# Kernel optimization log

Hardware: AMD Instinct MI355X
Metric: run time of the kernel (lower is better)

The kernel has to match this reference:

```python
import jax, jax.numpy as jnp
import numpy as np

N = 13627        # n_nodes (from negative_sampling call in source)
E_EDGES = 504378 # n_edges
F_IN = 64
H1, H2, LIN_H = 300, 100, 100  # CONFIG HIDDEN_1/HIDDEN_2/LINEAR_HIDDEN


def setup_inputs() -> dict:
    key = jax.random.key(0)
    ks = jax.random.split(key, 10)
    x = jax.random.normal(ks[0], (N, F_IN), jnp.float32)
    edge_index = jax.random.randint(ks[1], (2, E_EDGES), 0, N, dtype=jnp.int64)
    neg_edge_index = jax.random.randint(ks[2], (2, E_EDGES), 0, N, dtype=jnp.int64)
    def w(k, shape):
        return jax.random.normal(k, shape, jnp.float32) * 0.05
    return dict(
        x=x, edge_index=edge_index, neg_edge_index=neg_edge_index,
        W1=w(ks[3], (2, F_IN, H1)), b1=jnp.zeros((H1,), jnp.float32),
        W2=w(ks[4], (2, H1, H2)), b2=jnp.zeros((H2,), jnp.float32),
        W3=w(ks[5], (2, H2, 1)), b3=jnp.zeros((1,), jnp.float32),
        linW1=w(ks[6], (F_IN, LIN_H)), linb1=jnp.zeros((LIN_H,), jnp.float32),
        linW2=w(ks[7], (F_IN, LIN_H)), linb2=jnp.zeros((LIN_H,), jnp.float32),
        c1=jnp.array([0.5], jnp.float32), c2=jnp.array([0.5], jnp.float32),
    )


def _cheb_norm(edge_index, n):
    # PyG ChebConv sym normalization with lambda_max=2: Lhat = L - I,
    # off-diagonal entries -deg[src]^-1/2 * deg[dst]^-1/2, diagonal 0.
    src, dst = edge_index[0], edge_index[1]
    deg = jax.ops.segment_sum(jnp.ones(src.shape, jnp.float32), src, num_segments=n)
    dinv = jnp.where(deg > 0, jax.lax.rsqrt(jnp.maximum(deg, 1.0)), 0.0)
    return -dinv[src] * dinv[dst]


def _cheb_conv(x, W, b, src, dst, norm, n):
    # K=2: out = Tx0 @ W[0] + Tx1 @ W[1] + b, with Tx1 = Lhat @ x (gather-scale-scatter)
    tx1 = jax.ops.segment_sum(norm[:, None] * x[src], dst, num_segments=n)
    return x @ W[0] + tx1 @ W[1] + b


def reference(x, edge_index, neg_edge_index, W1, b1, W2, b2, W3, b3,
              linW1, linb1, linW2, linb2, c1, c2):
    n = x.shape[0]
    src, dst = edge_index[0], edge_index[1]
    norm = _cheb_norm(edge_index, n)
    h = jax.nn.relu(_cheb_conv(x, W1, b1, src, dst, norm, n))
    x1 = jax.nn.relu(_cheb_conv(h, W2, b2, src, dst, norm, n))
    xo = x1 + jax.nn.relu(x @ linW1 + linb1)
    z = x1 + jax.nn.relu(x @ linW2 + linb2)
    pos = jax.nn.sigmoid(jnp.sum(z[edge_index[0]] * z[edge_index[1]], axis=1))
    pos_loss = -jnp.mean(jnp.log(pos + 1e-15))
    neg = jax.nn.sigmoid(jnp.sum(z[neg_edge_index[0]] * z[neg_edge_index[1]], axis=1))
    neg_loss = -jnp.mean(jnp.log(1.0 - neg + 1e-15))
    r_loss = pos_loss + neg_loss
    out = _cheb_conv(xo, W3, b3, src, dst, norm, n)
    return out, r_loss, c1, c2
```

## Files before the change

### kernel.cpp

```cpp
#include <hip/hip_runtime.h>
#include <math.h>


typedef unsigned short ushort_t;
typedef float v2f __attribute__((ext_vector_type(2)));
typedef short bf16x8 __attribute__((ext_vector_type(8)));
typedef float f32x4 __attribute__((ext_vector_type(4)));

#define GBM 64
#define GBN 64
#define GBK 32
#define LDK 72
#define HB  256
#define PACKN 6816

__device__ inline short f2bf(float f) {
    unsigned u = __float_as_uint(f);
    u += 0x7fff + ((u >> 16) & 1);
    return (short)(u >> 16);
}
__device__ inline float bflo(unsigned w) { return __uint_as_float(w << 16); }
__device__ inline float bfhi(unsigned w) { return __uint_as_float(w & 0xffff0000u); }

__device__ inline float dot16fp8(uint4 ra, uint4 rb) {
    float dot = 0.0f;
    v2f fa, fb;
    fa = __builtin_amdgcn_cvt_pk_f32_fp8(ra.x, false);
    fb = __builtin_amdgcn_cvt_pk_f32_fp8(rb.x, false);
    dot += fa.x * fb.x + fa.y * fb.y;
    fa = __builtin_amdgcn_cvt_pk_f32_fp8(ra.x, true);
    fb = __builtin_amdgcn_cvt_pk_f32_fp8(rb.x, true);
    dot += fa.x * fb.x + fa.y * fb.y;
    fa = __builtin_amdgcn_cvt_pk_f32_fp8(ra.y, false);
    fb = __builtin_amdgcn_cvt_pk_f32_fp8(rb.y, false);
    dot += fa.x * fb.x + fa.y * fb.y;
    fa = __builtin_amdgcn_cvt_pk_f32_fp8(ra.y, true);
    fb = __builtin_amdgcn_cvt_pk_f32_fp8(rb.y, true);
    dot += fa.x * fb.x + fa.y * fb.y;
    fa = __builtin_amdgcn_cvt_pk_f32_fp8(ra.z, false);
    fb = __builtin_amdgcn_cvt_pk_f32_fp8(rb.z, false);
    dot += fa.x * fb.x + fa.y * fb.y;
    fa = __builtin_amdgcn_cvt_pk_f32_fp8(ra.z, true);
    fb = __builtin_amdgcn_cvt_pk_f32_fp8(rb.z, true);
    dot += fa.x * fb.x + fa.y * fb.y;
    fa = __builtin_amdgcn_cvt_pk_f32_fp8(ra.w, false);
    fb = __builtin_amdgcn_cvt_pk_f32_fp8(rb.w, false);
    dot += fa.x * fb.x + fa.y * fb.y;
    fa = __builtin_amdgcn_cvt_pk_f32_fp8(ra.w, true);
    fb = __builtin_amdgcn_cvt_pk_f32_fp8(rb.w, true);
    dot += fa.x * fb.x + fa.y * fb.y;
    return dot;
}

__global__ __launch_bounds__(512) void hist_both_pairs_kernel(
    const int* __restrict__ ei, const int* __restrict__ nei,
    int* __restrict__ degp, int* __restrict__ cntp,
    int2* __restrict__ pp, int2* __restrict__ pn, int E) {
    __shared__ int lhs[PACKN];
    __shared__ int lhd[PACKN];
    for (int i = threadIdx.x; i < PACKN; i += 512) { lhs[i] = 0; lhd[i] = 0; }
    __syncthreads();
    const int b = blockIdx.x;
    const int chunk = (E + HB - 1) / HB;
    const int e0 = b * chunk;
    const int e1 = (e0 + chunk < E) ? (e0 + chunk) : E;
    for (int e = e0 + threadIdx.x; e < e1; e += 512) {
        int s = ei[e], d = ei[E + e];
        atomicAdd(&lhs[s >> 1], 1 << ((s & 1) << 4));
        atomicAdd(&lhd[d >> 1], 1 << ((d & 1) << 4));
        pp[e] = make_int2(s, d);
        pn[e] = make_int2(nei[e], nei[E + e]);
    }
    __syncthreads();
    int* ds = degp + (size_t)b * PACKN;
    int* cs = cntp + (size_t)b * PACKN;
    for (int i = threadIdx.x; i < PACKN; i += 512) { ds[i] = lhs[i]; cs[i] = lhd[i]; }
}

__global__ void merge_kernel(const int* __restrict__ degp, const int* __restrict__ cntp,
                             ushort_t* __restrict__ off, int Nal,
                             float* __restrict__ dinv, int* __restrict__ rowptr,
                             float* __restrict__ acc, int n) {
    int v = blockIdx.x * blockDim.x + threadIdx.x;
    if (v == 0) {
        rowptr[0] = 0;
        acc[0] = 0.0f; acc[1] = 0.0f; acc[2] = 0.0f; acc[3] = 0.0f;
    }
    if (v >= n) return;
    const int vh = v >> 1, sh = (v & 1) << 4;
    int d = 0;
    for (int b = 0; b < HB; ++b)
        d += (degp[(size_t)b * PACKN + vh] >> sh) & 0xffff;
    dinv[v] = (d > 0) ? (1.0f / sqrtf((float)d)) : 0.0f;
    int run = 0;
    for (int b = 0; b < HB; ++b) {
        off[(size_t)b * Nal + v] = (ushort_t)run;
        run += (cntp[(size_t)b * PACKN + vh] >> sh) & 0xffff;
    }
    rowptr[v + 1] = run;
}

__global__ void scan_kernel(int* __restrict__ rowptr, int n) {
    __shared__ int wsum[16];
    __shared__ int carry_s;
    if (threadIdx.x == 0) carry_s = 0;
    __syncthreads();
    int nchunk = (n + 1023) / 1024;
    int wid = threadIdx.x >> 6, lane = threadIdx.x & 63;
    for (int c = 0; c < nchunk; ++c) {
        int i = c * 1024 + threadIdx.x;
        int v = (i < n) ? rowptr[i + 1] : 0;
        int s = v;
        for (int off = 1; off < 64; off <<= 1) {
            int t = __shfl_up(s, off, 64);
            if (lane >= off) s += t;
        }
        if (lane == 63) wsum[wid] = s;
        __syncthreads();
        if (wid == 0 && lane < 16) {
            int wsv = wsum[lane];
            for (int off = 1; off < 16; off <<= 1) {
                int t = __shfl_up(wsv, off, 64);
                if (lane >= off) wsv += t;
            }
            wsum[lane] = wsv;
        }
        __syncthreads();
        int base = carry_s + (wid > 0 ? wsum[wid - 1] : 0);
        int inc = base + s;
        if (i < n) rowptr[i + 1] = inc;
        __syncthreads();
        if (threadIdx.x == 1023) carry_s = inc;
        __syncthreads();
    }
}

__global__ __launch_bounds__(512) void fill_lds_kernel(
    const int* __restrict__ ei, const float* __restrict__ dinv,
    const int* __restrict__ rowptr, const ushort_t* __restrict__ off, int Nal,
    int* __restrict__ colidx, float* __restrict__ wnorm, int E) {
    __shared__ int lh[PACKN];
    for (int i = threadIdx.x; i < PACKN; i += 512) lh[i] = 0;
    __syncthreads();
    const int b = blockIdx.x;
    const int chunk = (E + HB - 1) / HB;
    const int e0 = b * chunk;
    const int e1 = (e0 + chunk < E) ? (e0 + chunk) : E;
    const ushort_t* boff = off + (size_t)b * Nal;
    for (int e = e0 + threadIdx.x; e < e1; e += 512) {
        int s = ei[e], d = ei[E + e];
        int sh = (d & 1) << 4;
        int old = atomicAdd(&lh[d >> 1], 1 << sh);
        int rank = (old >> sh) & 0xffff;
        int slot = rowptr[d] + (int)boff[d] + rank;
        colidx[slot] = s;
        wnorm[slot] = -dinv[s] * dinv[d];
    }
}

__global__ void xt_kernel(const float* __restrict__ x, const int* __restrict__ rowptr,
                          const int* __restrict__ colidx, const float* __restrict__ wnorm,
                          float* __restrict__ XT, int n) {
    int node = (blockIdx.x * blockDim.x + threadIdx.x) >> 6;
    if (node >= n) return;
    int lane = threadIdx.x & 63;
    int grp = lane >> 4;
    int l = lane & 15;
    int j0 = rowptr[node], j1 = rowptr[node + 1];
    float4 a = {0, 0, 0, 0};
    int j = j0 + grp;
    if (j < j1) {
        float w = wnorm[j];
        int c = colidx[j];
        float4 r = ((const float4*)(x + (size_t)c * 64))[l];
        for (;;) {
            int jn = j + 4;
            bool more = jn < j1;
            float wn = 0.0f;
            float4 rn = r;
            if (more) {
                int cn = colidx[jn];
                wn = wnorm[jn];
                rn = ((const float4*)(x + (size_t)cn * 64))[l];
            }
            a.x += w * r.x; a.y += w * r.y; a.z += w * r.z; a.w += w * r.w;
            if (!more) break;
            j = jn; w = wn; r = rn;
        }
    }
#pragma unroll
    for (int off = 16; off <= 32; off <<= 1) {
        a.x += __shfl_xor(a.x, off, 64);
        a.y += __shfl_xor(a.y, off, 64);
        a.z += __shfl_xor(a.z, off, 64);
        a.w += __shfl_xor(a.w, off, 64);
    }
    if (grp == 0) {
        float4 xv = ((const float4*)(x + (size_t)node * 64))[l];
        *(float4*)&XT[(size_t)node * 128 + l * 4] = xv;
        *(float4*)&XT[(size_t)node * 128 + 64 + l * 4] = a;
    }
}

__global__ __launch_bounds__(256) void gemm_mfma(
    const float* __restrict__ A, int lda,
    const float* __restrict__ B0, const float* __restrict__ B1,
    const float* __restrict__ bias0, const float* __restrict__ bias1,
    float* __restrict__ C, int ldc, ushort_t* __restrict__ Cbf,
    int Nrows, int K, int Ncols, int split, int relu) {
    __shared__ short As[GBM * LDK];
    __shared__ short Bs[GBN * LDK];
    const int bm = blockIdx.y * GBM, bn = blockIdx.x * GBN;
    const int tid = threadIdx.x;
    const int w = tid >> 6, l = tid & 63;
    const int wm = (w >> 1) * 32, wn = (w & 1) * 32;
    const int lr = l & 15;
    const int kg = l >> 4;
    const int arow = tid >> 2, aseg = tid & 3;
    const int bcol = tid & 63, bk2 = (tid >> 6) * 2;
    const int ldb0 = split, ldb1 = Ncols - split;

    const int arowg = bm + arow;
    const int bcolg = bn + bcol;
    const float* Bsrc = (bcolg < split) ? (B0 + bcolg)
                       : ((bcolg < Ncols) ? (B1 + (bcolg - split)) : nullptr);
    const int ldb = (bcolg < split) ? ldb0 : ldb1;

    f32x4 acc00 = {0,0,0,0}, acc01 = {0,0,0,0}, acc10 = {0,0,0,0}, acc11 = {0,0,0,0};

    for (int k0 = 0; k0 < K; k0 += GBK) {
        {
            int kk = k0 + aseg * 8;
            bf16x8 v;
            if (arowg < Nrows && kk + 7 < K) {
                float4 f0 = *(const float4*)&A[(size_t)arowg * lda + kk];
                float4 f1 = *(const float4*)&A[(size_t)arowg * lda + kk + 4];
                v[0] = f2bf(f0.x); v[1] = f2bf(f0.y); v[2] = f2bf(f0.z); v[3] = f2bf(f0.w);
                v[4] = f2bf(f1.x); v[5] = f2bf(f1.y); v[6] = f2bf(f1.z); v[7] = f2bf(f1.w);
            } else {
#pragma unroll
                for (int i = 0; i < 8; ++i)
                    v[i] = (arowg < Nrows && kk + i < K)
                         ? f2bf(A[(size_t)arowg * lda + kk + i]) : (short)0;
            }
            *(bf16x8*)&As[arow * LDK + aseg * 8] = v;
        }
#pragma unroll
        for (int q = 0; q < 4; ++q) {
            int k = q * 8 + bk2;
            unsigned pw = 0u;
            if (Bsrc) {
                float f0 = (k0 + k < K) ? Bsrc[(size_t)(k0 + k) * ldb] : 0.0f;
                float f1 = (k0 + k + 1 < K) ? Bsrc[(size_t)(k0 + k + 1) * ldb] : 0.0f;
                pw = (unsigned)(unsigned short)f2bf(f0)
                   | ((unsigned)(unsigned short)f2bf(f1) << 16);
            }
            *(unsigned*)&Bs[bcol * LDK + k] = pw;
        }
        __syncthreads();
        bf16x8 a0 = *(const bf16x8*)&As[(wm + lr) * LDK + kg * 8];
        bf16x8 a1 = *(const bf16x8*)&As[(wm + 16 + lr) * LDK + kg * 8];
        bf16x8 b0 = *(const bf16x8*)&Bs[(wn + lr) * LDK + kg * 8];
        bf16x8 b1 = *(const bf16x8*)&Bs[(wn + 16 + lr) * LDK + kg * 8];
        acc00 = __builtin_amdgcn_mfma_f32_16x16x32_bf16(a0, b0, acc00, 0, 0, 0);
        acc01 = __builtin_amdgcn_mfma_f32_16x16x32_bf16(a0, b1, acc01, 0, 0, 0);
        acc10 = __builtin_amdgcn_mfma_f32_16x16x32_bf16(a1, b0, acc10, 0, 0, 0);
        acc11 = __builtin_amdgcn_mfma_f32_16x16x32_bf16(a1, b1, acc11, 0, 0, 0);
        __syncthreads();
    }
#pragma unroll
    for (int i = 0; i < 2; ++i) {
        int rbase = bm + wm + i * 16 + kg * 4;
#pragma unroll
        for (int j = 0; j < 2; ++j) {
            int col = bn + wn + j * 16 + lr;
            if (col >= Ncols) continue;
            float bv = (col < split) ? (bias0 ? bias0[col] : 0.0f)
                                     : (bias1 ? bias1[col - split] : 0.0f);
            f32x4 a = (i == 0) ? (j == 0 ? acc00 : acc01) : (j == 0 ? acc10 : acc11);
#pragma unroll
            for (int r = 0; r < 4; ++r) {
                int row = rbase + r;
                if (row >= Nrows) continue;
                float o = a[r] + bv;
                if (relu) o = fmaxf(o, 0.0f);
                if (col < split || !Cbf)
                    C[(size_t)row * ldc + col] = o;
                else
                    Cbf[(size_t)row * 128 + (col - split)] = (ushort_t)f2bf(o);
            }
        }
    }
}

__global__ void segsum_combine1_kernel(const ushort_t* __restrict__ hb,
                                       const int* __restrict__ rowptr, const int* __restrict__ colidx,
                                       const float* __restrict__ wnorm,
                                       const float* __restrict__ G2a, const float* __restrict__ b2,
                                       float* __restrict__ x1, int n) {
    int node = (blockIdx.x * blockDim.x + threadIdx.x) >> 6;
    if (node >= n) return;
    int lane = threadIdx.x & 63;
    int grp = lane >> 4;
    int l = lane & 15;
    int j0 = rowptr[node], j1 = rowptr[node + 1];
    float acc[8] = {};
    int j = j0 + grp;
    if (j < j1) {
        float w = wnorm[j];
        int c = colidx[j];
        uint4 r = ((const uint4*)(hb + (size_t)c * 128))[l];
        for (;;) {
            int jn = j + 4;
            bool more = jn < j1;
            float wn = 0.0f;
            uint4 rn = r;
            if (more) {
                int cn = colidx[jn];
                wn = wnorm[jn];
                rn = ((const uint4*)(hb + (size_t)cn * 128))[l];
            }
            acc[0] += w * bflo(r.x); acc[1] += w * bfhi(r.x);
            acc[2] += w * bflo(r.y); acc[3] += w * bfhi(r.y);
            acc[4] += w * bflo(r.z); acc[5] += w * bfhi(r.z);
            acc[6] += w * bflo(r.w); acc[7] += w * bfhi(r.w);
            if (!more) break;
            j = jn; w = wn; r = rn;
        }
    }
#pragma unroll
    for (int k = 0; k < 8; ++k) {
        acc[k] += __shfl_xor(acc[k], 16, 64);
        acc[k] += __shfl_xor(acc[k], 32, 64);
    }
    if (grp == 0) {
        int f = l * 8;
        if (f < 100) {
            float4 g0 = *(const float4*)&G2a[(size_t)node * 100 + f];
            float4 bv0 = *(const float4*)&b2[f];
            float4 o0;
            o0.x = fmaxf(g0.x + acc[0] + bv0.x, 0.0f);
            o0.y = fmaxf(g0.y + acc[1] + bv0.y, 0.0f);
            o0.z = fmaxf(g0.z + acc[2] + bv0.z, 0.0f);
            o0.w = fmaxf(g0.w + acc[3] + bv0.w, 0.0f);
            *(float4*)&x1[(size_t)node * 100 + f] = o0;
            if (f + 8 <= 100) {
                float4 g1 = *(const float4*)&G2a[(size_t)node * 100 + f + 4];
                float4 bv1 = *(const float4*)&b2[f + 4];
                float4 o1;
                o1.x = fmaxf(g1.x + acc[4] + bv1.x, 0.0f);
                o1.y = fmaxf(g1.y + acc[5] + bv1.y, 0.0f);
                o1.z = fmaxf(g1.z + acc[6] + bv1.z, 0.0f);
                o1.w = fmaxf(g1.w + acc[7] + bv1.w, 0.0f);
                *(float4*)&x1[(size_t)node * 100 + f + 4] = o1;
            }
        }
    }
}

__global__ void combine2_kernel(const float* __restrict__ S, const float* __restrict__ x1,
                                const float* __restrict__ w3b,
                                float* __restrict__ xo, unsigned* __restrict__ zf,
                                float* __restrict__ sv, int n) {
    int idx = blockIdx.x * blockDim.x + threadIdx.x;
    if (idx >= n * 32) return;
    int i = idx >> 5, q = idx & 31;
    unsigned w = 0u;
    float part = 0.0f;
    if (q < 25) {
        float4 s1 = *(const float4*)&S[(size_t)i * 200 + q * 4];
        float4 s2 = *(const float4*)&S[(size_t)i * 200 + 100 + q * 4];
        float4 xv = *(const float4*)&x1[(size_t)i * 100 + q * 4];
        float4 a, b;
        a.x = xv.x + fmaxf(s1.x, 0.0f); a.y = xv.y + fmaxf(s1.y, 0.0f);
        a.z = xv.z + fmaxf(s1.z, 0.0f); a.w = xv.w + fmaxf(s1.w, 0.0f);
        b.x = xv.x + fmaxf(s2.x, 0.0f); b.y = xv.y + fmaxf(s2.y, 0.0f);
        b.z = xv.z + fmaxf(s2.z, 0.0f); b.w = xv.w + fmaxf(s2.w, 0.0f);
        *(float4*)&xo[(size_t)i * 100 + q * 4] = a;
        w = (unsigned)__builtin_amdgcn_cvt_pk_fp8_f32(b.x, b.y, 0, false);
        w = (unsigned)__builtin_amdgcn_cvt_pk_fp8_f32(b.z, b.w, (int)w, true);
        float4 wv = *(const float4*)&w3b[q * 4];
        part = a.x * wv.x + a.y * wv.y + a.z * wv.z + a.w * wv.w;
    }
    zf[(size_t)i * 32 + q] = w;
#pragma unroll
    for (int off = 16; off > 0; off >>= 1)
        part += __shfl_xor(part, off, 32);
    if (q == 0) sv[i] = part;
}

__global__ __launch_bounds__(256) void edge_loss_fp8_kernel(
    const unsigned* __restrict__ zf, const int2* __restrict__ pp,
    const int2* __restrict__ pn, int E, float* __restrict__ accv) {
    const int y = blockIdx.y;
    const int2* __restrict__ pairs = y ? pn : pp;
    const int l = threadIdx.x & 7;
    const int g = (blockIdx.x * blockDim.x + threadIdx.x) >> 3;
    const int ng = (gridDim.x * blockDim.x) >> 3;
    const int stride2 = 2 * ng;
    float s = 0.0f;
    const int gA = g, gB = g + ng;
    int niterA = (gA < E) ? ((E - 1 - gA) / stride2 + 1) : 0;
    int niterB = (gB < E) ? ((E - 1 - gB) / stride2 + 1) : 0;
    if (niterA > 0) {
        int eB0 = (gB < E) ? gB : (E - 1);
        int eA1 = (gA + stride2 < E) ? (gA + stride2) : (E - 1);
        int eB1 = (gB + stride2 < E) ? (gB + stride2) : (E - 1);
        int2 pA0 = pairs[gA], pB0 = pairs[eB0];
        int2 pA1 = pairs[eA1], pB1 = pairs[eB1];
        uint4 raA = *(const uint4*)&zf[(size_t)pA0.x * 32 + l * 4];
        uint4 rbA = *(const uint4*)&zf[(size_t)pA0.y * 32 + l * 4];
        uint4 raB = *(const uint4*)&zf[(size_t)pB0.x * 32 + l * 4];
        uint4 rbB = *(const uint4*)&zf[(size_t)pB0.y * 32 + l * 4];
        for (int t = 0; t < niterA; ++t) {
            int eA2 = gA + (t + 2) * stride2; eA2 = (eA2 < E) ? eA2 : (E - 1);
            int eB2 = gB + (t + 2) * stride2; eB2 = (eB2 < E) ? eB2 : (E - 1);
            int2 pA2 = pairs[eA2], pB2 = pairs[eB2];
            uint4 raA1 = *(const uint4*)&zf[(size_t)pA1.x * 32 + l * 4];
            uint4 rbA1 = *(const uint4*)&zf[(size_t)pA1.y * 32 + l * 4];
            uint4 raB1 = *(const uint4*)&zf[(size_t)pB1.x * 32 + l * 4];
            uint4 rbB1 = *(const uint4*)&zf[(size_t)pB1.y * 32 + l * 4];
            float dA = dot16fp8(raA, rbA);
            float dB = dot16fp8(raB, rbB);
            dA += __shfl_xor(dA, 1, 8); dB += __shfl_xor(dB, 1, 8);
            dA += __shfl_xor(dA, 2, 8); dB += __shfl_xor(dB, 2, 8);
            dA += __shfl_xor(dA, 4, 8); dB += __shfl_xor(dB, 4, 8);
            if (l == 0) {
                float sgA = 1.0f / (1.0f + expf(-dA));
                s += y ? logf(1.0f - sgA + 1e-15f) : logf(sgA + 1e-15f);
                if (t < niterB) {
                    float sgB = 1.0f / (1.0f + expf(-dB));
                    s += y ? logf(1.0f - sgB + 1e-15f) : logf(sgB + 1e-15f);
                }
            }
            pA1 = pA2; pB1 = pB2;
            raA = raA1; rbA = rbA1; raB = raB1; rbB = rbB1;
        }
    }
    __shared__ float red[256];
    red[threadIdx.x] = s;
    __syncthreads();
    for (int st = 128; st > 0; st >>= 1) {
        if (threadIdx.x < st) red[threadIdx.x] += red[threadIdx.x + st];
        __syncthreads();
    }
    if (threadIdx.x == 0) atomicAdd(&accv[y], red[0]);
}

__global__ void out_finalize_kernel(const float* __restrict__ xo, const float* __restrict__ W3,
                                    const float* __restrict__ b3, const int* __restrict__ rowptr,
                                    const int* __restrict__ colidx, const float* __restrict__ wnorm,
                                    const float* __restrict__ sv, const float* __restrict__ accv,
                                    const float* __restrict__ c1, const float* __restrict__ c2,
                                    float* __restrict__ out, int n, int E) {
    int i = blockIdx.x * blockDim.x + threadIdx.x;
    if (i == 0) {
        out[n]     = -(accv[0] + accv[1]) / (float)E;
        out[n + 1] = c1[0];
        out[n + 2] = c2[0];
    }
    if (i >= n) return;
    const float4* a = (const float4*)(xo + (size_t)i * 100);
    const float4* wv = (const float4*)W3;
    float acc = b3[0];
#pragma unroll
    for (int q = 0; q < 25; ++q) {
        float4 va = a[q], vw = wv[q];
        acc += va.x * vw.x + va.y * vw.y + va.z * vw.z + va.w * vw.w;
    }
    int j1 = rowptr[i + 1];
    for (int j = rowptr[i]; j < j1; ++j)
        acc += wnorm[j] * sv[colidx[j]];
    out[i] = acc;
}

extern "C" void kernel_launch(void* const* d_in, const int* in_sizes, int n_in,
                              void* d_out, int out_size, void* d_ws, size_t ws_size,
                              hipStream_t stream) {
    (void)n_in; (void)out_size; (void)ws_size;
    const float* x   = (const float*)d_in[0];
    const int*   ei  = (const int*)d_in[1];
    const int*   nei = (const int*)d_in[2];
    const float* W1  = (const float*)d_in[3];
    const float* b1  = (const float*)d_in[4];
    const float* W2  = (const float*)d_in[5];
    const float* b2  = (const float*)d_in[6];
    const float* W3  = (const float*)d_in[7];
    const float* b3  = (const float*)d_in[8];
    const float* lw1 = (const float*)d_in[9];
    const float* lb1 = (const float*)d_in[10];
    const float* lw2 = (const float*)d_in[11];
    const float* lb2 = (const float*)d_in[12];
    const float* c1  = (const float*)d_in[13];
    const float* c2  = (const float*)d_in[14];

    const int Nn = in_sizes[0] / 64;
    const int E  = in_sizes[1] / 2;

    const size_t Nal = ((size_t)Nn + 5) & ~(size_t)3;
    const size_t Eal = ((size_t)E + 3) & ~(size_t)3;

    float* ws       = (float*)d_ws;
    float* acc      = ws;
    float* dinv     = acc + 4;
    int*   rowptr   = (int*)(dinv + Nal);
    int*   colidx   = rowptr + Nal;
    float* wnorm    = (float*)(colidx + Eal);
    int2*  pp       = (int2*)(wnorm + Eal);
    int2*  pn       = pp + Eal;
    int*   degp     = (int*)(pn + Eal);
    int*   cntp     = degp + (size_t)HB * PACKN;
    ushort_t* offus = (ushort_t*)(cntp + (size_t)HB * PACKN);
    float* XT       = (float*)(offus + (size_t)HB * Nal);
    float* h        = XT + (size_t)Nn * 128;
    float* G2a      = h  + (size_t)Nn * 300;
    float* x1       = G2a + (size_t)Nn * 100;
    float* xo       = x1 + (size_t)Nn * 100;
    size_t zoff     = (size_t)(xo + (size_t)Nn * 100 - ws);
    zoff = (zoff + 31) & ~(size_t)31;
    unsigned* zf    = (unsigned*)(ws + zoff);
    size_t hoff     = zoff + (size_t)Nn * 32 + 63;
    hoff &= ~(size_t)63;
    ushort_t* hWb   = (ushort_t*)(ws + hoff);
    float* sv       = ws + hoff + (size_t)Nn * 64;
    float* S        = h;

    const int MB = (Nn + GBM - 1) / GBM;

    hist_both_pairs_kernel<<<HB, 512, 0, stream>>>(ei, nei, degp, cntp, pp, pn, E);
    merge_kernel<<<(Nn + 255) / 256, 256, 0, stream>>>(degp, cntp, offus, (int)Nal,
                                                       dinv, rowptr, acc, Nn);
    scan_kernel<<<1, 1024, 0, stream>>>(rowptr, Nn);
    fill_lds_kernel<<<HB, 512, 0, stream>>>(ei, dinv, rowptr, offus, (int)Nal,
                                            colidx, wnorm, E);

    xt_kernel<<<(Nn + 3) / 4, 256, 0, stream>>>(x, rowptr, colidx, wnorm, XT, Nn);
    gemm_mfma<<<dim3(5, MB), 256, 0, stream>>>(
        XT, 128, W1, nullptr, b1, nullptr, h, 300, nullptr, Nn, 128, 300, 300, 1);

    gemm_mfma<<<dim3(4, MB), 256, 0, stream>>>(
        h, 300, W2, W2 + 300 * 100, nullptr, nullptr, G2a, 100, hWb, Nn, 300, 200, 100, 0);
    segsum_combine1_kernel<<<(Nn + 3) / 4, 256, 0, stream>>>(hWb, rowptr, colidx, wnorm,
                                                             G2a, b2, x1, Nn);

    gemm_mfma<<<dim3(4, MB), 256, 0, stream>>>(
        x, 64, lw1, lw2, lb1, lb2, S, 200, nullptr, Nn, 64, 200, 100, 0);
    combine2_kernel<<<(Nn * 32 + 255) / 256, 256, 0, stream>>>(S, x1, W3 + 100,
                                                               xo, zf, sv, Nn);

    edge_loss_fp8_kernel<<<dim3(1024, 2), 256, 0, stream>>>(zf, pp, pn, E, acc);

    out_finalize_kernel<<<(Nn + 255) / 256, 256, 0, stream>>>(
        xo, W3, b3, rowptr, colidx, wnorm, sv, acc, c1, c2, (float*)d_out, Nn, E);
}
```

Baseline: 240.3 us.

## Store activations in bf16, parallelize merge, read edge lists directly in loss

Converts x to bf16 once in the histogram kernel and keeps XT and the first hidden layer h in bf16 (padded leading dimension 304), so the GEMMs load bf16 directly instead of converting fp32 each time. The merge kernel splits each node's 256 partial histograms across four threads with shuffle reductions and scans. The pair-packing writes are removed, and the edge loss kernel reads the original src/dst arrays with two separate loads per edge. These cut memory traffic and conversion work, at the cost of extra bf16 rounding in the Lhat@x aggregation and less coalesced index loads in the loss kernel.

```diff
diff --git a/kernel.cpp b/kernel.cpp
--- a/kernel.cpp
+++ b/kernel.cpp
@@ -52,10 +52,10 @@
     return dot;
 }
 
-__global__ __launch_bounds__(512) void hist_both_pairs_kernel(
-    const int* __restrict__ ei, const int* __restrict__ nei,
+__global__ __launch_bounds__(512) void hist_both_x_kernel(
+    const int* __restrict__ ei, const float* __restrict__ x,
     int* __restrict__ degp, int* __restrict__ cntp,
-    int2* __restrict__ pp, int2* __restrict__ pn, int E) {
+    ushort_t* __restrict__ xb, int Nn, int E) {
     __shared__ int lhs[PACKN];
     __shared__ int lhd[PACKN];
     for (int i = threadIdx.x; i < PACKN; i += 512) { lhs[i] = 0; lhd[i] = 0; }
@@ -68,36 +68,50 @@
         int s = ei[e], d = ei[E + e];
         atomicAdd(&lhs[s >> 1], 1 << ((s & 1) << 4));
         atomicAdd(&lhd[d >> 1], 1 << ((d & 1) << 4));
-        pp[e] = make_int2(s, d);
-        pn[e] = make_int2(nei[e], nei[E + e]);
     }
     __syncthreads();
     int* ds = degp + (size_t)b * PACKN;
     int* cs = cntp + (size_t)b * PACKN;
     for (int i = threadIdx.x; i < PACKN; i += 512) { ds[i] = lhs[i]; cs[i] = lhd[i]; }
+    const int rpb = (Nn + HB - 1) / HB;
+    const int r0 = b * rpb;
+    const int r1 = (r0 + rpb < Nn) ? (r0 + rpb) : Nn;
+    for (int i = r0 * 64 + (int)threadIdx.x; i < r1 * 64; i += 512)
+        xb[i] = (ushort_t)f2bf(x[i]);
 }
 
 __global__ void merge_kernel(const int* __restrict__ degp, const int* __restrict__ cntp,
                              ushort_t* __restrict__ off, int Nal,
                              float* __restrict__ dinv, int* __restrict__ rowptr,
                              float* __restrict__ acc, int n) {
-    int v = blockIdx.x * blockDim.x + threadIdx.x;
-    if (v == 0) {
+    int tid = blockIdx.x * blockDim.x + threadIdx.x;
+    if (tid == 0) {
         rowptr[0] = 0;
         acc[0] = 0.0f; acc[1] = 0.0f; acc[2] = 0.0f; acc[3] = 0.0f;
     }
+    int v = tid >> 2, qq = tid & 3;
     if (v >= n) return;
     const int vh = v >> 1, sh = (v & 1) << 4;
-    int d = 0;
-    for (int b = 0; b < HB; ++b)
-        d += (degp[(size_t)b * PACKN + vh] >> sh) & 0xffff;
-    dinv[v] = (d > 0) ? (1.0f / sqrtf((float)d)) : 0.0f;
-    int run = 0;
-    for (int b = 0; b < HB; ++b) {
+    const int b0 = qq * (HB / 4), b1 = b0 + HB / 4;
+    int dsum = 0, csum = 0;
+    for (int b = b0; b < b1; ++b) {
+        dsum += (degp[(size_t)b * PACKN + vh] >> sh) & 0xffff;
+        csum += (cntp[(size_t)b * PACKN + vh] >> sh) & 0xffff;
+    }
+    int dtot = dsum;
+    dtot += __shfl_xor(dtot, 1, 64);
+    dtot += __shfl_xor(dtot, 2, 64);
+    int inc = csum;
+    int t = __shfl_up(inc, 1, 64); if (qq >= 1) inc += t;
+    t = __shfl_up(inc, 2, 64);     if (qq >= 2) inc += t;
+    int ex = inc - csum;
+    if (qq == 0) dinv[v] = (dtot > 0) ? (1.0f / sqrtf((float)dtot)) : 0.0f;
+    if (qq == 3) rowptr[v + 1] = inc;
+    int run = ex;
+    for (int b = b0; b < b1; ++b) {
         off[(size_t)b * Nal + v] = (ushort_t)run;
         run += (cntp[(size_t)b * PACKN + vh] >> sh) & 0xffff;
     }
-    rowptr[v + 1] = run;
 }
 
 __global__ void scan_kernel(int* __restrict__ rowptr, int n) {
@@ -158,56 +172,57 @@
     }
 }
 
-__global__ void xt_kernel(const float* __restrict__ x, const int* __restrict__ rowptr,
+__global__ void xt_kernel(const ushort_t* __restrict__ xb, const int* __restrict__ rowptr,
                           const int* __restrict__ colidx, const float* __restrict__ wnorm,
-                          float* __restrict__ XT, int n) {
+                          ushort_t* __restrict__ XTb, int n) {
     int node = (blockIdx.x * blockDim.x + threadIdx.x) >> 6;
     if (node >= n) return;
     int lane = threadIdx.x & 63;
     int grp = lane >> 4;
     int l = lane & 15;
     int j0 = rowptr[node], j1 = rowptr[node + 1];
-    float4 a = {0, 0, 0, 0};
+    float a0 = 0, a1 = 0, a2 = 0, a3 = 0;
     int j = j0 + grp;
     if (j < j1) {
         float w = wnorm[j];
         int c = colidx[j];
-        float4 r = ((const float4*)(x + (size_t)c * 64))[l];
+        uint2 r = ((const uint2*)(xb + (size_t)c * 64))[l];
         for (;;) {
             int jn = j + 4;
             bool more = jn < j1;
             float wn = 0.0f;
-            float4 rn = r;
+            uint2 rn = r;
             if (more) {
                 int cn = colidx[jn];
                 wn = wnorm[jn];
-                rn = ((const float4*)(x + (size_t)cn * 64))[l];
-            }
-            a.x += w * r.x; a.y += w * r.y; a.z += w * r.z; a.w += w * r.w;
+                rn = ((const uint2*)(xb + (size_t)cn * 64))[l];
+            }
+            a0 += w * bflo(r.x); a1 += w * bfhi(r.x);
+            a2 += w * bflo(r.y); a3 += w * bfhi(r.y);
             if (!more) break;
             j = jn; w = wn; r = rn;
         }
     }
-#pragma unroll
-    for (int off = 16; off <= 32; off <<= 1) {
-        a.x += __shfl_xor(a.x, off, 64);
-        a.y += __shfl_xor(a.y, off, 64);
-        a.z += __shfl_xor(a.z, off, 64);
-        a.w += __shfl_xor(a.w, off, 64);
-    }
+    a0 += __shfl_xor(a0, 16, 64); a0 += __shfl_xor(a0, 32, 64);
+    a1 += __shfl_xor(a1, 16, 64); a1 += __shfl_xor(a1, 32, 64);
+    a2 += __shfl_xor(a2, 16, 64); a2 += __shfl_xor(a2, 32, 64);
+    a3 += __shfl_xor(a3, 16, 64); a3 += __shfl_xor(a3, 32, 64);
     if (grp == 0) {
-        float4 xv = ((const float4*)(x + (size_t)node * 64))[l];
-        *(float4*)&XT[(size_t)node * 128 + l * 4] = xv;
-        *(float4*)&XT[(size_t)node * 128 + 64 + l * 4] = a;
+        uint2 xv = ((const uint2*)(xb + (size_t)node * 64))[l];
+        *(uint2*)&XTb[(size_t)node * 128 + l * 4] = xv;
+        uint2 p;
+        p.x = (unsigned)(unsigned short)f2bf(a0) | ((unsigned)(unsigned short)f2bf(a1) << 16);
+        p.y = (unsigned)(unsigned short)f2bf(a2) | ((unsigned)(unsigned short)f2bf(a3) << 16);
+        *(uint2*)&XTb[(size_t)node * 128 + 64 + l * 4] = p;
     }
 }
 
 __global__ __launch_bounds__(256) void gemm_mfma(
-    const float* __restrict__ A, int lda,
+    const float* __restrict__ A, const ushort_t* __restrict__ Abf, int lda,
     const float* __restrict__ B0, const float* __restrict__ B1,
     const float* __restrict__ bias0, const float* __restrict__ bias1,
-    float* __restrict__ C, int ldc, ushort_t* __restrict__ Cbf,
-    int Nrows, int K, int Ncols, int split, int relu) {
+    float* __restrict__ C, int ldc, ushort_t* __restrict__ Cbf, int ldcbf,
+    int cbf_mode, int Nrows, int K, int Ncols, int split, int relu) {
     __shared__ short As[GBM * LDK];
     __shared__ short Bs[GBN * LDK];
     const int bm = blockIdx.y * GBM, bn = blockIdx.x * GBN;
@@ -232,7 +247,16 @@
         {
             int kk = k0 + aseg * 8;
             bf16x8 v;
-            if (arowg < Nrows && kk + 7 < K) {
+            if (Abf) {
+                if (arowg < Nrows && kk + 7 < K) {
+                    v = *(const bf16x8*)&Abf[(size_t)arowg * lda + kk];
+                } else {
+#pragma unroll
+                    for (int i = 0; i < 8; ++i)
+                        v[i] = (arowg < Nrows && kk + i < K)
+                             ? (short)Abf[(size_t)arowg * lda + kk + i] : (short)0;
+                }
+            } else if (arowg < Nrows && kk + 7 < K) {
                 float4 f0 = *(const float4*)&A[(size_t)arowg * lda + kk];
                 float4 f1 = *(const float4*)&A[(size_t)arowg * lda + kk + 4];
                 v[0] = f2bf(f0.x); v[1] = f2bf(f0.y); v[2] = f2bf(f0.z); v[3] = f2bf(f0.w);
@@ -284,10 +308,12 @@
                 if (row >= Nrows) continue;
                 float o = a[r] + bv;
                 if (relu) o = fmaxf(o, 0.0f);
-                if (col < split || !Cbf)
+                if (cbf_mode == 2)
+                    Cbf[(size_t)row * ldcbf + col] = (ushort_t)f2bf(o);
+                else if (cbf_mode == 1 && col >= split)
+                    Cbf[(size_t)row * 128 + (col - split)] = (ushort_t)f2bf(o);
+                else
                     C[(size_t)row * ldc + col] = o;
-                else
-                    Cbf[(size_t)row * 128 + (col - split)] = (ushort_t)f2bf(o);
             }
         }
     }
@@ -390,10 +416,10 @@
 }
 
 __global__ __launch_bounds__(256) void edge_loss_fp8_kernel(
-    const unsigned* __restrict__ zf, const int2* __restrict__ pp,
-    const int2* __restrict__ pn, int E, float* __restrict__ accv) {
+    const unsigned* __restrict__ zf, const int* __restrict__ ei,
+    const int* __restrict__ nei, int E, float* __restrict__ accv) {
     const int y = blockIdx.y;
-    const int2* __restrict__ pairs = y ? pn : pp;
+    const int* __restrict__ lst = y ? nei : ei;
     const int l = threadIdx.x & 7;
     const int g = (blockIdx.x * blockDim.x + threadIdx.x) >> 3;
     const int ng = (gridDim.x * blockDim.x) >> 3;
@@ -406,20 +432,23 @@
         int eB0 = (gB < E) ? gB : (E - 1);
         int eA1 = (gA + stride2 < E) ? (gA + stride2) : (E - 1);
         int eB1 = (gB + stride2 < E) ? (gB + stride2) : (E - 1);
-        int2 pA0 = pairs[gA], pB0 = pairs[eB0];
-        int2 pA1 = pairs[eA1], pB1 = pairs[eB1];
-        uint4 raA = *(const uint4*)&zf[(size_t)pA0.x * 32 + l * 4];
-        uint4 rbA = *(const uint4*)&zf[(size_t)pA0.y * 32 + l * 4];
-        uint4 raB = *(const uint4*)&zf[(size_t)pB0.x * 32 + l * 4];
-        uint4 rbB = *(const uint4*)&zf[(size_t)pB0.y * 32 + l * 4];
+        int aA0 = lst[gA], bA0 = lst[E + gA];
+        int aB0 = lst[eB0], bB0 = lst[E + eB0];
+        int aA1 = lst[eA1], bA1 = lst[E + eA1];
+        int aB1 = lst[eB1], bB1 = lst[E + eB1];
+        uint4 raA = *(const uint4*)&zf[(size_t)aA0 * 32 + l * 4];
+        uint4 rbA = *(const uint4*)&zf[(size_t)bA0 * 32 + l * 4];
+        uint4 raB = *(const uint4*)&zf[(size_t)aB0 * 32 + l * 4];
+        uint4 rbB = *(const uint4*)&zf[(size_t)bB0 * 32 + l * 4];
         for (int t = 0; t < niterA; ++t) {
             int eA2 = gA + (t + 2) * stride2; eA2 = (eA2 < E) ? eA2 : (E - 1);
             int eB2 = gB + (t + 2) * stride2; eB2 = (eB2 < E) ? eB2 : (E - 1);
-            int2 pA2 = pairs[eA2], pB2 = pairs[eB2];
-            uint4 raA1 = *(const uint4*)&zf[(size_t)pA1.x * 32 + l * 4];
-            uint4 rbA1 = *(const uint4*)&zf[(size_t)pA1.y * 32 + l * 4];
-            uint4 raB1 = *(const uint4*)&zf[(size_t)pB1.x * 32 + l * 4];
-            uint4 rbB1 = *(const uint4*)&zf[(size_t)pB1.y * 32 + l * 4];
+            int aA2 = lst[eA2], bA2 = lst[E + eA2];
+            int aB2 = lst[eB2], bB2 = lst[E + eB2];
+            uint4 raA1 = *(const uint4*)&zf[(size_t)aA1 * 32 + l * 4];
+            uint4 rbA1 = *(const uint4*)&zf[(size_t)bA1 * 32 + l * 4];
+            uint4 raB1 = *(const uint4*)&zf[(size_t)aB1 * 32 + l * 4];
+            uint4 rbB1 = *(const uint4*)&zf[(size_t)bB1 * 32 + l * 4];
             float dA = dot16fp8(raA, rbA);
             float dB = dot16fp8(raB, rbB);
             dA += __shfl_xor(dA, 1, 8); dB += __shfl_xor(dB, 1, 8);
@@ -433,7 +462,7 @@
                     s += y ? logf(1.0f - sgB + 1e-15f) : logf(sgB + 1e-15f);
                 }
             }
-            pA1 = pA2; pB1 = pB2;
+            aA1 = aA2; bA1 = bA2; aB1 = aB2; bB1 = bB2;
             raA = raA1; rbA = rbA1; raB = raB1; rbB = rbB1;
         }
     }
@@ -499,6 +528,7 @@
 
     const size_t Nal = ((size_t)Nn + 5) & ~(size_t)3;
     const size_t Eal = ((size_t)E + 3) & ~(size_t)3;
+    const int LDH = 304;
 
     float* ws       = (float*)d_ws;
     float* acc      = ws;
@@ -506,49 +536,50 @@
     int*   rowptr   = (int*)(dinv + Nal);
     int*   colidx   = rowptr + Nal;
     float* wnorm    = (float*)(colidx + Eal);
-    int2*  pp       = (int2*)(wnorm + Eal);
-    int2*  pn       = pp + Eal;
-    int*   degp     = (int*)(pn + Eal);
+    int*   degp     = (int*)(wnorm + Eal);
     int*   cntp     = degp + (size_t)HB * PACKN;
     ushort_t* offus = (ushort_t*)(cntp + (size_t)HB * PACKN);
-    float* XT       = (float*)(offus + (size_t)HB * Nal);
-    float* h        = XT + (size_t)Nn * 128;
-    float* G2a      = h  + (size_t)Nn * 300;
+    ushort_t* xb    = offus + (size_t)HB * Nal;
+    ushort_t* XTb   = xb + (size_t)Nn * 64;
+    ushort_t* hb    = XTb + (size_t)Nn * 128;
+    float* G2a      = (float*)(hb + (size_t)Nn * LDH);
     float* x1       = G2a + (size_t)Nn * 100;
     float* xo       = x1 + (size_t)Nn * 100;
-    size_t zoff     = (size_t)(xo + (size_t)Nn * 100 - ws);
+    float* S        = xo + (size_t)Nn * 100;
+    size_t zoff     = (size_t)(S + (size_t)Nn * 200 - ws);
     zoff = (zoff + 31) & ~(size_t)31;
     unsigned* zf    = (unsigned*)(ws + zoff);
-    size_t hoff     = zoff + (size_t)Nn * 32 + 63;
-    hoff &= ~(size_t)63;
-    ushort_t* hWb   = (ushort_t*)(ws + hoff);
-    float* sv       = ws + hoff + (size_t)Nn * 64;
-    float* S        = h;
-
+    size_t hoff2    = zoff + (size_t)Nn * 32 + 63;
+    hoff2 &= ~(size_t)63;
+    ushort_t* hWb   = (ushort_t*)(ws + hoff2);
+    float* sv       = ws + hoff2 + (size_t)Nn * 64;
     const int MB = (Nn + GBM - 1) / GBM;
 
-    hist_both_pairs_kernel<<<HB, 512, 0, stream>>>(ei, nei, degp, cntp, pp, pn, E);
-    merge_kernel<<<(Nn + 255) / 256, 256, 0, stream>>>(degp, cntp, offus, (int)Nal,
-                                                       dinv, rowptr, acc, Nn);
+    hist_both_x_kernel<<<HB, 512, 0, stream>>>(ei, x, degp, cntp, xb, Nn, E);
+    merge_kernel<<<(4 * Nn + 255) / 256, 256, 0, stream>>>(degp, cntp, offus, (int)Nal,
+                                                           dinv, rowptr, acc, Nn);
     scan_kernel<<<1, 1024, 0, stream>>>(rowptr, Nn);
     fill_lds_kernel<<<HB, 512, 0, stream>>>(ei, dinv, rowptr, offus, (int)Nal,
                                             colidx, wnorm, E);
 
-    xt_kernel<<<(Nn + 3) / 4, 256, 0, stream>>>(x, rowptr, colidx, wnorm, XT, Nn);
+    xt_kernel<<<(Nn + 3) / 4, 256, 0, stream>>>(xb, rowptr, colidx, wnorm, XTb, Nn);
     gemm_mfma<<<dim3(5, MB), 256, 0, stream>>>(
-        XT, 128, W1, nullptr, b1, nullptr, h, 300, nullptr, Nn, 128, 300, 300, 1);
+        nullptr, XTb, 128, W1, nullptr, b1, nullptr,
+        nullptr, 0, hb, LDH, 2, Nn, 128, 300, 300, 1);
 
     gemm_mfma<<<dim3(4, MB), 256, 0, stream>>>(
-        h, 300, W2, W2 + 300 * 100, nullptr, nullptr, G2a, 100, hWb, Nn, 300, 200, 100, 0);
+        nullptr, hb, LDH, W2, W2 + 300 * 100, nullptr, nullptr,
+        G2a, 100, hWb, 0, 1, Nn, 300, 200, 100, 0);
     segsum_combine1_kernel<<<(Nn + 3) / 4, 256, 0, stream>>>(hWb, rowptr, colidx, wnorm,
                                                              G2a, b2, x1, Nn);
 
     gemm_mfma<<<dim3(4, MB), 256, 0, stream>>>(
-        x, 64, lw1, lw2, lb1, lb2, S, 200, nullptr, Nn, 64, 200, 100, 0);
+        nullptr, xb, 64, lw1, lw2, lb1, lb2,
+        S, 200, nullptr, 0, 0, Nn, 64, 200, 100, 0);
     combine2_kernel<<<(Nn * 32 + 255) / 256, 256, 0, stream>>>(S, x1, W3 + 100,
                                                                xo, zf, sv, Nn);
 
-    edge_loss_fp8_kernel<<<dim3(1024, 2), 256, 0, stream>>>(zf, pp, pn, E, acc);
+    edge_loss_fp8_kernel<<<dim3(1024, 2), 256, 0, stream>>>(zf, ei, nei, E, acc);
 
     out_finalize_kernel<<<(Nn + 255) / 256, 256, 0, stream>>>(
         xo, W3, b3, rowptr, colidx, wnorm, sv, acc, c1, c2, (float*)d_out, Nn, E);
```

Result: faster. 215.1 us (-10.5%).
